# Kernel tuning notes

Hardware: AMD Instinct MI355X
Metric: run time of the kernel (lower is better)

## Reference

```python
import jax, jax.numpy as jnp
import numpy as np

D_MODEL = 1024
N_HEAD = 16
DIM_PER_HEAD = D_MODEL // N_HEAD
B, S = 8, 1024


def setup_inputs() -> dict:
    key = jax.random.key(0)
    ks = jax.random.split(key, 12)
    s = 0.02
    return {
        "k": jax.random.normal(ks[0], (B, S, D_MODEL), jnp.float32),
        "v": jax.random.normal(ks[1], (B, S, D_MODEL), jnp.float32),
        "q": jax.random.normal(ks[2], (B, S, D_MODEL), jnp.float32),
        "attn_mask": jax.random.randint(ks[3], (B, S, S), 0, 2, jnp.int32),
        "Wk": jax.random.normal(ks[4], (D_MODEL, D_MODEL), jnp.float32) * s,
        "bk": jnp.zeros((D_MODEL,), jnp.float32),
        "Wv": jax.random.normal(ks[5], (D_MODEL, D_MODEL), jnp.float32) * s,
        "bv": jnp.zeros((D_MODEL,), jnp.float32),
        "Wq": jax.random.normal(ks[6], (D_MODEL, D_MODEL), jnp.float32) * s,
        "bq": jnp.zeros((D_MODEL,), jnp.float32),
        "Wo": jax.random.normal(ks[7], (D_MODEL, D_MODEL), jnp.float32) * s,
        "bo": jnp.zeros((D_MODEL,), jnp.float32),
    }


def reference(k, v, q, attn_mask, Wk, bk, Wv, bv, Wq, bq, Wo, bo):
    batch, key_len, _ = k.shape
    query_len = q.shape[1]
    scale = 1.0 / jnp.sqrt(jnp.float32(DIM_PER_HEAD))

    def split_heads(x):  # [b, s, d] -> [b, h, s, dh]
        return x.reshape(batch, -1, N_HEAD, DIM_PER_HEAD).transpose(0, 2, 1, 3)

    key_up = split_heads(k @ Wk + bk)
    value_up = split_heads(v @ Wv + bv)
    query_up = split_heads(q @ Wq + bq) * scale

    # [b, h, q, k] scores; mask nonzero entries with -inf (masked_fill_ semantics)
    scores = jnp.einsum("bhqd,bhkd->bhqk", query_up, key_up)
    scores = jnp.where(attn_mask[:, None, :, :] != 0, -jnp.inf, scores)
    attn = jax.nn.softmax(scores, axis=-1)
    # NOTE: original applies dropout but discards the result; attn (pre-dropout) is used.
    context = jnp.einsum("bhqk,bhkd->bhqd", attn, value_up)
    context = context.transpose(0, 2, 1, 3).reshape(batch, query_len, D_MODEL)
    output = context @ Wo + bo
    attn_mean = attn.sum(axis=1) / N_HEAD  # [b, q, k]
    return output, attn_mean
```

## Files before the change

kernel.cpp:

```cpp
#include <hip/hip_runtime.h>
#include <hip/hip_bf16.h>

typedef unsigned short u16;
typedef unsigned int u32;
typedef __attribute__((ext_vector_type(8))) short bf16x8;
typedef __attribute__((ext_vector_type(4))) float f32x4;
typedef __attribute__((ext_vector_type(4))) u16 u16x4;
typedef __attribute__((ext_vector_type(4))) u32 u32x4;

#define DEV static __device__ __forceinline__

DEV u16 f2bf(float x) {
  unsigned u = __builtin_bit_cast(unsigned, x);
  u += 0x7fffu + ((u >> 16) & 1u);
  return (u16)(u >> 16);
}
DEV float bf2f(u16 u) { return __builtin_bit_cast(float, ((unsigned)u) << 16); }

DEV u32 cvtpk(float lo, float hi) {
  u32 r;
  asm("v_cvt_pk_bf16_f32 %0, %1, %2" : "=v"(r) : "v"(lo), "v"(hi));
  return r;
}

DEV void glds16(const u16* g, u16* l) {
  __builtin_amdgcn_global_load_lds(
      (const __attribute__((address_space(1))) void*)g,
      (__attribute__((address_space(3))) void*)l, 16, 0, 0);
}

__global__ __launch_bounds__(256) void xcvt(
    const float* __restrict__ k, const float* __restrict__ v,
    const float* __restrict__ q, u16* __restrict__ Xb) {
  const size_t i0 = (size_t)blockIdx.x * 256 + threadIdx.x;
  for (size_t t = i0; t < 6291456; t += 524288) {
    const size_t e = t * 4;
    const float* src = (e < 8388608) ? k + e
                     : (e < 16777216) ? v + (e - 8388608)
                     : q + (e - 16777216);
    const f32x4 x = *(const f32x4*)src;
    u16x4 o;
#pragma unroll
    for (int r = 0; r < 4; ++r) o[r] = f2bf(x[r]);
    *(u16x4*)&Xb[e] = o;
  }
}

__global__ __launch_bounds__(256) void transpose_w(
    const float* __restrict__ w0, const float* __restrict__ w1,
    const float* __restrict__ w2, const float* __restrict__ w3,
    u16* __restrict__ out) {
  __shared__ u16 tile[32][33];
  const int mat = blockIdx.y;
  const float* in = (mat == 0) ? w0 : (mat == 1) ? w1 : (mat == 2) ? w2 : w3;
  u16* o = out + (size_t)mat * 1048576;
  const int bk = ((int)blockIdx.x & 31) << 5;
  const int bn = ((int)blockIdx.x >> 5) << 5;
  const int tx = threadIdx.x & 31, ty = threadIdx.x >> 5;
#pragma unroll
  for (int i = 0; i < 32; i += 8)
    tile[ty + i][tx] = f2bf(in[(size_t)(bk + ty + i) * 1024 + bn + tx]);
  __syncthreads();
#pragma unroll
  for (int i = 0; i < 32; i += 8)
    o[(size_t)(bn + ty + i) * 1024 + bk + tx] = tile[tx][ty + i];
}

__global__ __launch_bounds__(256) void maskpack(
    const int* __restrict__ mask, unsigned long long* __restrict__ Mb) {
  const int qt = blockIdx.x, b = blockIdx.y;
  const int tid = threadIdx.x;
  const int w = tid >> 6, l = tid & 63;
  const int ln = l & 15, lg = l >> 4;
  const int* Mp = mask + ((size_t)b << 20) + ((size_t)(qt << 4) << 10);
  unsigned long long m = 0ull;
#pragma unroll
  for (int t = 0; t < 16; ++t) {
    const int key = (w << 8) + (t << 4) + ln;
#pragma unroll
    for (int r = 0; r < 4; ++r) {
      const int row = (lg << 2) + r;
      if (Mp[((size_t)row << 10) + key] != 0) m |= 1ull << ((t << 2) + r);
    }
  }
  Mb[((((size_t)b << 6) + qt) << 8) + tid] = m;
}

__global__ __launch_bounds__(256) void gemm_qkv(
    const u16* __restrict__ Xb, const u16* __restrict__ WTall,
    const float* __restrict__ bK, const float* __restrict__ bV,
    const float* __restrict__ bQ,
    u16* __restrict__ Kup, u16* __restrict__ VupT, u16* __restrict__ Qup) {
  __shared__ u16 As[4096];
  __shared__ u16 Bs[4096];
  const int mode = blockIdx.y;
  const u16* A = Xb + (size_t)mode * 8388608;
  const u16* Bw = WTall + (size_t)mode * 1048576;
  const float* bias = (mode == 0) ? bK : (mode == 1) ? bV : bQ;

  const int tid = threadIdx.x;
  const int w = tid >> 6, l = tid & 63;
  const int ln = l & 15, lg = l >> 4, kg8 = lg << 3;
  const int wr = w >> 1, wc = w & 1;
  const int mb = ((int)blockIdx.x >> 3) << 7;
  const int nb = ((int)blockIdx.x & 7) << 7;

  const int srow = (w << 5) + (l >> 2);
  const int sseg = (l & 3) << 3;
  const u16* Ag0 = A + (size_t)(mb + srow) * 1024 + sseg;
  const u16* Bg0 = Bw + (size_t)(nb + srow) * 1024 + sseg;
  u16* Al0 = As + srow * 32 + sseg;
  u16* Bl0 = Bs + srow * 32 + sseg;

  f32x4 acc[4][4] = {};
  const int ar = (wr << 6) + ln;
  const int br = (wc << 6) + ln;

  for (int k0 = 0; k0 < 1024; k0 += 32) {
    glds16(Ag0 + k0, Al0);
    glds16(Ag0 + 16384 + k0, Al0 + 512);
    glds16(Bg0 + k0, Bl0);
    glds16(Bg0 + 16384 + k0, Bl0 + 512);
    __syncthreads();
    bf16x8 aa[4], bb[4];
#pragma unroll
    for (int mt = 0; mt < 4; ++mt) aa[mt] = *(const bf16x8*)&As[(ar + (mt << 4)) * 32 + kg8];
#pragma unroll
    for (int nt = 0; nt < 4; ++nt) bb[nt] = *(const bf16x8*)&Bs[(br + (nt << 4)) * 32 + kg8];
#pragma unroll
    for (int mt = 0; mt < 4; ++mt)
#pragma unroll
      for (int nt = 0; nt < 4; ++nt)
        acc[mt][nt] = __builtin_amdgcn_mfma_f32_16x16x32_bf16(aa[mt], bb[nt], acc[mt][nt], 0, 0, 0);
    __syncthreads();
  }

  const float scale = (mode == 2) ? 0.125f : 1.0f;
#pragma unroll
  for (int mt = 0; mt < 4; ++mt) {
    const int m0 = mb + (wr << 6) + (mt << 4) + (lg << 2);
    const int bb_ = m0 >> 10, s0 = m0 & 1023;
#pragma unroll
    for (int nt = 0; nt < 4; ++nt) {
      const int n = nb + (wc << 6) + (nt << 4) + ln;
      const float bval = bias[n];
      const int h = n >> 6, dh = n & 63;
      const size_t bh = (size_t)(bb_ * 16 + h);
      if (mode == 1) {
        const int wv = dh >> 4, lnv = dh & 15;
        const int kk = s0 >> 5, lgv = (s0 >> 3) & 3, e0 = s0 & 7;
        u16x4 pk;
#pragma unroll
        for (int r = 0; r < 4; ++r) pk[r] = f2bf(acc[mt][nt][r] + bval);
        *(u16x4*)&VupT[(bh << 16) + (wv << 14) + (kk << 9) + (lgv << 7) +
                       (lnv << 3) + e0] = pk;
      } else if (mode == 0) {
        const int half = dh >> 5, lg2 = (dh >> 3) & 3, e = dh & 7;
        const int T = s0 >> 4;
        u16* base = Kup + (bh << 16) + (T << 10) + (half << 9) + (lg2 << 7) + e;
#pragma unroll
        for (int r = 0; r < 4; ++r)
          base[((s0 & 15) + r) << 3] = f2bf(acc[mt][nt][r] + bval);
      } else {
#pragma unroll
        for (int r = 0; r < 4; ++r)
          Qup[((bh << 10) + s0 + r) * 64 + dh] =
              f2bf((acc[mt][nt][r] + bval) * scale);
      }
    }
  }
}

__global__ __launch_bounds__(256) void gemm_out(
    const u16* __restrict__ Ctx, const u16* __restrict__ WTall,
    const float* __restrict__ bO, float* __restrict__ Out) {
  __shared__ u16 As[4096];
  __shared__ u16 Bs[4096];
  const u16* Bw = WTall + 3145728;

  const int tid = threadIdx.x;
  const int w = tid >> 6, l = tid & 63;
  const int ln = l & 15, lg = l >> 4, kg8 = lg << 3;
  const int wr = w >> 1, wc = w & 1;
  const int mb = ((int)blockIdx.x >> 3) << 7;
  const int nb = ((int)blockIdx.x & 7) << 7;

  const int srow = (w << 5) + (l >> 2);
  const int sseg = (l & 3) << 3;
  const u16* Ag0 = Ctx + (size_t)(mb + srow) * 1024 + sseg;
  const u16* Bg0 = Bw + (size_t)(nb + srow) * 1024 + sseg;
  u16* Al0 = As + srow * 32 + sseg;
  u16* Bl0 = Bs + srow * 32 + sseg;

  f32x4 acc[4][4] = {};
  const int ar = (wr << 6) + ln;
  const int br = (wc << 6) + ln;

  for (int k0 = 0; k0 < 1024; k0 += 32) {
    glds16(Ag0 + k0, Al0);
    glds16(Ag0 + 16384 + k0, Al0 + 512);
    glds16(Bg0 + k0, Bl0);
    glds16(Bg0 + 16384 + k0, Bl0 + 512);
    __syncthreads();
    bf16x8 aa[4], bb[4];
#pragma unroll
    for (int mt = 0; mt < 4; ++mt) aa[mt] = *(const bf16x8*)&As[(ar + (mt << 4)) * 32 + kg8];
#pragma unroll
    for (int nt = 0; nt < 4; ++nt) bb[nt] = *(const bf16x8*)&Bs[(br + (nt << 4)) * 32 + kg8];
#pragma unroll
    for (int mt = 0; mt < 4; ++mt)
#pragma unroll
      for (int nt = 0; nt < 4; ++nt)
        acc[mt][nt] = __builtin_amdgcn_mfma_f32_16x16x32_bf16(aa[mt], bb[nt], acc[mt][nt], 0, 0, 0);
    __syncthreads();
  }
#pragma unroll
  for (int mt = 0; mt < 4; ++mt) {
    const int m0 = mb + (wr << 6) + (mt << 4) + (lg << 2);
#pragma unroll
    for (int nt = 0; nt < 4; ++nt) {
      const int n = nb + (wc << 6) + (nt << 4) + ln;
      const float bval = bO[n];
#pragma unroll
      for (int r = 0; r < 4; ++r)
        Out[(size_t)(m0 + r) * 1024 + n] = acc[mt][nt][r] + bval;
    }
  }
}

__global__ __launch_bounds__(256, 2) void attn_kernel(
    const u16* __restrict__ Qup, const u16* __restrict__ Kf,
    const u16* __restrict__ Vf, const unsigned long long* __restrict__ Mb,
    u16* __restrict__ Ctx, float* __restrict__ Am) {
  __shared__ u16 P_lds[16 * 1024];
  __shared__ float red_s[4][16];
  __shared__ float invs[16];

  const int tid = threadIdx.x;
  const int w = tid >> 6, l = tid & 63;
  const int ln = l & 15, lg = l >> 4;
  const int kg8 = lg << 3;

  const int bid = (int)blockIdx.x;
  const int b = bid & 7;
  const int qt = bid >> 3;
  const int qb = qt << 4;

  const unsigned long long mbits = Mb[((((size_t)b << 6) + qt) << 8) + tid];

  u32x4 accp[8];

#pragma unroll 1
  for (int hh = 0; hh < 16; ++hh) {
    const size_t bh = (size_t)(b * 16 + hh);
    const u16* Qp = Qup + ((bh << 10) + qb) * 64;
    const u16* Kb = Kf + (bh << 16);
    const u16* Vb = Vf + (bh << 16) + ((size_t)w << 14);

    const bf16x8 qa0 = *(const bf16x8*)&Qp[ln * 64 + kg8];
    const bf16x8 qa1 = *(const bf16x8*)&Qp[ln * 64 + 32 + kg8];

    bf16x8 ka[3], kb[3];
#pragma unroll
    for (int p = 0; p < 3; ++p) {
      const int To = ((w << 4) + p) << 10;
      ka[p] = *(const bf16x8*)&Kb[To + (l << 3)];
      kb[p] = *(const bf16x8*)&Kb[To + 512 + (l << 3)];
    }

    float rsum[4] = {0, 0, 0, 0};
#pragma unroll
    for (int t = 0; t < 16; ++t) {
      const int s = t % 3;
      const bf16x8 k0 = ka[s], k1 = kb[s];
      if (t + 3 < 16) {
        const int To = ((w << 4) + t + 3) << 10;
        ka[s] = *(const bf16x8*)&Kb[To + (l << 3)];
        kb[s] = *(const bf16x8*)&Kb[To + 512 + (l << 3)];
      }
      f32x4 c = {0, 0, 0, 0};
      c = __builtin_amdgcn_mfma_f32_16x16x32_bf16(qa0, k0, c, 0, 0, 0);
      c = __builtin_amdgcn_mfma_f32_16x16x32_bf16(qa1, k1, c, 0, 0, 0);
      const int key = (w << 8) + (t << 4) + ln;
      float p[4];
#pragma unroll
      for (int r = 0; r < 4; ++r) {
        p[r] = ((mbits >> ((t << 2) + r)) & 1ull) ? 0.0f : __expf(c[r] - 4.0f);
        rsum[r] += p[r];
      }
      const u32 pk01 = cvtpk(p[0], p[1]);
      const u32 pk23 = cvtpk(p[2], p[3]);
      const int r0 = lg << 2;
      *(u16*)((char*)P_lds + ((((r0 + 0) << 11) + (key << 1)) ^ (((r0 + 0) & 7) << 4))) = (u16)pk01;
      *(u16*)((char*)P_lds + ((((r0 + 1) << 11) + (key << 1)) ^ (((r0 + 1) & 7) << 4))) = (u16)(pk01 >> 16);
      *(u16*)((char*)P_lds + ((((r0 + 2) << 11) + (key << 1)) ^ (((r0 + 2) & 7) << 4))) = (u16)pk23;
      *(u16*)((char*)P_lds + ((((r0 + 3) << 11) + (key << 1)) ^ (((r0 + 3) & 7) << 4))) = (u16)(pk23 >> 16);
    }
#pragma unroll
    for (int off = 1; off < 16; off <<= 1) {
#pragma unroll
      for (int r = 0; r < 4; ++r) rsum[r] += __shfl_xor(rsum[r], off);
    }
    if (ln == 0) {
#pragma unroll
      for (int r = 0; r < 4; ++r) red_s[w][(lg << 2) + r] = rsum[r];
    }

    bf16x8 vr[4];
#pragma unroll
    for (int p = 0; p < 4; ++p)
      vr[p] = *(const bf16x8*)&Vb[(p << 9) + (l << 3)];

    __syncthreads();
    float inv[4];
#pragma unroll
    for (int r = 0; r < 4; ++r) {
      const int row = (lg << 2) + r;
      inv[r] = 1.0f / (red_s[0][row] + red_s[1][row] + red_s[2][row] + red_s[3][row]);
    }
    if (ln == 0) {
#pragma unroll
      for (int r = 0; r < 4; ++r) invs[(lg << 2) + r] = inv[r];
    }

    f32x4 c0 = {0, 0, 0, 0}, c1 = {0, 0, 0, 0};
#pragma unroll
    for (int kk = 0; kk < 32; ++kk) {
      const int s = kk & 3;
      const bf16x8 vb = vr[s];
      if (kk + 4 < 32)
        vr[s] = *(const bf16x8*)&Vb[((kk + 4) << 9) + (l << 3)];
      const int a0 = ((ln << 11) + (((kk << 5) + kg8) << 1)) ^ ((ln & 7) << 4);
      const bf16x8 pa = *(const bf16x8*)((const char*)P_lds + a0);
      if (kk & 1)
        c1 = __builtin_amdgcn_mfma_f32_16x16x32_bf16(pa, vb, c1, 0, 0, 0);
      else
        c0 = __builtin_amdgcn_mfma_f32_16x16x32_bf16(pa, vb, c0, 0, 0, 0);
    }
    {
      const u32 q01 = cvtpk((c0[0] + c1[0]) * inv[0], (c0[1] + c1[1]) * inv[1]);
      const u32 q23 = cvtpk((c0[2] + c1[2]) * inv[2], (c0[3] + c1[3]) * inv[3]);
      u16* Cp = &Ctx[(((size_t)b << 10) + qb + (lg << 2)) * 1024 + (hh << 6) + (w << 4) + ln];
      Cp[0] = (u16)q01;
      Cp[1024] = (u16)(q01 >> 16);
      Cp[2048] = (u16)q23;
      Cp[3072] = (u16)(q23 >> 16);
    }

    {
      const int row = tid >> 4;
      const float iv = invs[row];
#pragma unroll
      for (int i = 0; i < 8; ++i) {
        const int chunk = (tid & 15) + (i << 4);
        const int bo_ = ((row << 11) + (chunk << 4)) ^ ((row & 7) << 4);
        const u32x4 pu = *(const u32x4*)((const char*)P_lds + bo_);
        u32x4 o;
#pragma unroll
        for (int j = 0; j < 4; ++j) {
          const float plo = __builtin_bit_cast(float, pu[j] << 16) * iv;
          const float phi = __builtin_bit_cast(float, pu[j] & 0xFFFF0000u) * iv;
          if (hh == 0) {
            o[j] = cvtpk(plo, phi);
          } else {
            const u32 a = accp[i][j];
            const float alo = __builtin_bit_cast(float, a << 16);
            const float ahi = __builtin_bit_cast(float, a & 0xFFFF0000u);
            o[j] = cvtpk(alo + plo, ahi + phi);
          }
        }
        accp[i] = o;
      }
    }
    __syncthreads();
  }

  {
    const int row = tid >> 4;
    float* Ag = Am + (((size_t)b << 10) + qb + row) * 1024;
#pragma unroll
    for (int i = 0; i < 8; ++i) {
      const int chunk = (tid & 15) + (i << 4);
      f32x4 o0, o1;
#pragma unroll
      for (int j = 0; j < 4; ++j) {
        const float lo = __builtin_bit_cast(float, accp[i][j] << 16) * 0.0625f;
        const float hi = __builtin_bit_cast(float, accp[i][j] & 0xFFFF0000u) * 0.0625f;
        if (j < 2) { o0[2 * j] = lo; o0[2 * j + 1] = hi; }
        else       { o1[2 * (j - 2)] = lo; o1[2 * (j - 2) + 1] = hi; }
      }
      *(f32x4*)&Ag[chunk << 3] = o0;
      *(f32x4*)&Ag[(chunk << 3) + 4] = o1;
    }
  }
}

extern "C" void kernel_launch(void* const* d_in, const int* in_sizes, int n_in,
                              void* d_out, int out_size, void* d_ws, size_t ws_size,
                              hipStream_t stream) {
  const float* k_in = (const float*)d_in[0];
  const float* v_in = (const float*)d_in[1];
  const float* q_in = (const float*)d_in[2];
  const int* mask = (const int*)d_in[3];
  const float* Wk = (const float*)d_in[4];
  const float* bk = (const float*)d_in[5];
  const float* Wv = (const float*)d_in[6];
  const float* bv = (const float*)d_in[7];
  const float* Wq = (const float*)d_in[8];
  const float* bq = (const float*)d_in[9];
  const float* Wo = (const float*)d_in[10];
  const float* bo = (const float*)d_in[11];

  float* out = (float*)d_out;
  float* amean = out + (size_t)8 * 1024 * 1024;

  u16* ws = (u16*)d_ws;
  u16* WT = ws;
  u16* Xb = ws + 4194304;
  unsigned long long* Mb = (unsigned long long*)(ws + 29360128);
  u16* Kf   = ws + 71303168;
  u16* Vf   = ws + 79691776;
  u16* Qup  = ws + 88080384;
  u16* Ctx  = ws + 96468992;

  xcvt<<<2048, 256, 0, stream>>>(k_in, v_in, q_in, Xb);
  transpose_w<<<dim3(1024, 4), dim3(256), 0, stream>>>(Wk, Wv, Wq, Wo, WT);
  maskpack<<<dim3(64, 8), dim3(256), 0, stream>>>(mask, Mb);
  gemm_qkv<<<dim3(512, 3), dim3(256), 0, stream>>>(
      Xb, WT, bk, bv, bq, Kf, Vf, Qup);
  attn_kernel<<<dim3(512), dim3(256), 0, stream>>>(
      Qup, Kf, Vf, Mb, Ctx, amean);
  gemm_out<<<512, 256, 0, stream>>>(Ctx, WT, bo, out);
}
```

Baseline: 297.1 us.

## Double-buffer P in LDS and prefetch next head's K/Q across iterations

The per-head probability tile, row sums and inverse sums now live in two alternating LDS buffers. This allows the trailing block barrier at the end of each head iteration to be removed. The next head's K and Q fragments are loaded before the mid-iteration barrier, so their global latency overlaps with the PV phase. The PV MFMA loop is also wrapped in raised wave priority. The cost is LDS use doubling to about 64KB per block and more live registers, which may limit occupancy under the two-blocks-per-CU launch bound.

```diff
diff --git a/kernel.cpp b/kernel.cpp
--- a/kernel.cpp
+++ b/kernel.cpp
@@ -232,9 +232,9 @@
     const u16* __restrict__ Qup, const u16* __restrict__ Kf,
     const u16* __restrict__ Vf, const unsigned long long* __restrict__ Mb,
     u16* __restrict__ Ctx, float* __restrict__ Am) {
-  __shared__ u16 P_lds[16 * 1024];
-  __shared__ float red_s[4][16];
-  __shared__ float invs[16];
+  __shared__ u16 P_lds[2][16384];
+  __shared__ float red_s[2][4][16];
+  __shared__ float invs[2][16];
 
   const int tid = threadIdx.x;
   const int w = tid >> 6, l = tid & 63;
@@ -250,23 +250,27 @@
 
   u32x4 accp[8];
 
+  bf16x8 ka[3], kb[3], qa0, qa1;
+  {
+    const size_t bh0 = (size_t)(b * 16);
+    const u16* Kb0 = Kf + (bh0 << 16);
+    const u16* Qp0 = Qup + ((bh0 << 10) + qb) * 64;
+#pragma unroll
+    for (int p = 0; p < 3; ++p) {
+      const int To = ((w << 4) + p) << 10;
+      ka[p] = *(const bf16x8*)&Kb0[To + (l << 3)];
+      kb[p] = *(const bf16x8*)&Kb0[To + 512 + (l << 3)];
+    }
+    qa0 = *(const bf16x8*)&Qp0[ln * 64 + kg8];
+    qa1 = *(const bf16x8*)&Qp0[ln * 64 + 32 + kg8];
+  }
+
 #pragma unroll 1
   for (int hh = 0; hh < 16; ++hh) {
+    const int pb_ = hh & 1;
     const size_t bh = (size_t)(b * 16 + hh);
-    const u16* Qp = Qup + ((bh << 10) + qb) * 64;
     const u16* Kb = Kf + (bh << 16);
     const u16* Vb = Vf + (bh << 16) + ((size_t)w << 14);
-
-    const bf16x8 qa0 = *(const bf16x8*)&Qp[ln * 64 + kg8];
-    const bf16x8 qa1 = *(const bf16x8*)&Qp[ln * 64 + 32 + kg8];
-
-    bf16x8 ka[3], kb[3];
-#pragma unroll
-    for (int p = 0; p < 3; ++p) {
-      const int To = ((w << 4) + p) << 10;
-      ka[p] = *(const bf16x8*)&Kb[To + (l << 3)];
-      kb[p] = *(const bf16x8*)&Kb[To + 512 + (l << 3)];
-    }
 
     float rsum[4] = {0, 0, 0, 0};
 #pragma unroll
@@ -291,10 +295,11 @@
       const u32 pk01 = cvtpk(p[0], p[1]);
       const u32 pk23 = cvtpk(p[2], p[3]);
       const int r0 = lg << 2;
-      *(u16*)((char*)P_lds + ((((r0 + 0) << 11) + (key << 1)) ^ (((r0 + 0) & 7) << 4))) = (u16)pk01;
-      *(u16*)((char*)P_lds + ((((r0 + 1) << 11) + (key << 1)) ^ (((r0 + 1) & 7) << 4))) = (u16)(pk01 >> 16);
-      *(u16*)((char*)P_lds + ((((r0 + 2) << 11) + (key << 1)) ^ (((r0 + 2) & 7) << 4))) = (u16)pk23;
-      *(u16*)((char*)P_lds + ((((r0 + 3) << 11) + (key << 1)) ^ (((r0 + 3) & 7) << 4))) = (u16)(pk23 >> 16);
+      char* Pb = (char*)P_lds + (pb_ << 15);
+      *(u16*)(Pb + ((((r0 + 0) << 11) + (key << 1)) ^ (((r0 + 0) & 7) << 4))) = (u16)pk01;
+      *(u16*)(Pb + ((((r0 + 1) << 11) + (key << 1)) ^ (((r0 + 1) & 7) << 4))) = (u16)(pk01 >> 16);
+      *(u16*)(Pb + ((((r0 + 2) << 11) + (key << 1)) ^ (((r0 + 2) & 7) << 4))) = (u16)pk23;
+      *(u16*)(Pb + ((((r0 + 3) << 11) + (key << 1)) ^ (((r0 + 3) & 7) << 4))) = (u16)(pk23 >> 16);
     }
 #pragma unroll
     for (int off = 1; off < 16; off <<= 1) {
@@ -303,7 +308,7 @@
     }
     if (ln == 0) {
 #pragma unroll
-      for (int r = 0; r < 4; ++r) red_s[w][(lg << 2) + r] = rsum[r];
+      for (int r = 0; r < 4; ++r) red_s[pb_][w][(lg << 2) + r] = rsum[r];
     }
 
     bf16x8 vr[4];
@@ -311,19 +316,35 @@
     for (int p = 0; p < 4; ++p)
       vr[p] = *(const bf16x8*)&Vb[(p << 9) + (l << 3)];
 
+    if (hh < 15) {
+      const size_t bhn = bh + 1;
+      const u16* Kbn = Kf + (bhn << 16);
+      const u16* Qpn = Qup + ((bhn << 10) + qb) * 64;
+#pragma unroll
+      for (int p = 0; p < 3; ++p) {
+        const int To = ((w << 4) + p) << 10;
+        ka[p] = *(const bf16x8*)&Kbn[To + (l << 3)];
+        kb[p] = *(const bf16x8*)&Kbn[To + 512 + (l << 3)];
+      }
+      qa0 = *(const bf16x8*)&Qpn[ln * 64 + kg8];
+      qa1 = *(const bf16x8*)&Qpn[ln * 64 + 32 + kg8];
+    }
+
     __syncthreads();
     float inv[4];
 #pragma unroll
     for (int r = 0; r < 4; ++r) {
       const int row = (lg << 2) + r;
-      inv[r] = 1.0f / (red_s[0][row] + red_s[1][row] + red_s[2][row] + red_s[3][row]);
+      inv[r] = 1.0f / (red_s[pb_][0][row] + red_s[pb_][1][row] +
+                       red_s[pb_][2][row] + red_s[pb_][3][row]);
     }
     if (ln == 0) {
 #pragma unroll
-      for (int r = 0; r < 4; ++r) invs[(lg << 2) + r] = inv[r];
+      for (int r = 0; r < 4; ++r) invs[pb_][(lg << 2) + r] = inv[r];
     }
 
     f32x4 c0 = {0, 0, 0, 0}, c1 = {0, 0, 0, 0};
+    __builtin_amdgcn_s_setprio(1);
 #pragma unroll
     for (int kk = 0; kk < 32; ++kk) {
       const int s = kk & 3;
@@ -331,12 +352,13 @@
       if (kk + 4 < 32)
         vr[s] = *(const bf16x8*)&Vb[((kk + 4) << 9) + (l << 3)];
       const int a0 = ((ln << 11) + (((kk << 5) + kg8) << 1)) ^ ((ln & 7) << 4);
-      const bf16x8 pa = *(const bf16x8*)((const char*)P_lds + a0);
+      const bf16x8 pa = *(const bf16x8*)((const char*)P_lds + (pb_ << 15) + a0);
       if (kk & 1)
         c1 = __builtin_amdgcn_mfma_f32_16x16x32_bf16(pa, vb, c1, 0, 0, 0);
       else
         c0 = __builtin_amdgcn_mfma_f32_16x16x32_bf16(pa, vb, c0, 0, 0, 0);
     }
+    __builtin_amdgcn_s_setprio(0);
     {
       const u32 q01 = cvtpk((c0[0] + c1[0]) * inv[0], (c0[1] + c1[1]) * inv[1]);
       const u32 q23 = cvtpk((c0[2] + c1[2]) * inv[2], (c0[3] + c1[3]) * inv[3]);
@@ -349,12 +371,12 @@
 
     {
       const int row = tid >> 4;
-      const float iv = invs[row];
+      const float iv = invs[pb_][row];
 #pragma unroll
       for (int i = 0; i < 8; ++i) {
         const int chunk = (tid & 15) + (i << 4);
         const int bo_ = ((row << 11) + (chunk << 4)) ^ ((row & 7) << 4);
-        const u32x4 pu = *(const u32x4*)((const char*)P_lds + bo_);
+        const u32x4 pu = *(const u32x4*)((const char*)P_lds + (pb_ << 15) + bo_);
         u32x4 o;
 #pragma unroll
         for (int j = 0; j < 4; ++j) {
@@ -372,7 +394,6 @@
         accp[i] = o;
       }
     }
-    __syncthreads();
   }
 
   {
```

After: 326.0 us. +9.7%, slower.

## Split attention heads across two blocks and combine partial attention means

Applied to the files above, without the earlier changes.

Each attention block now processes 8 of the 16 heads rather than all of them, which doubles the grid from 512 to 1024 blocks and gives the 256-CU GPU more parallelism. Each half writes its bf16 partial sum of attention probabilities to a workspace buffer. A new combine kernel adds the two partials, scales by 1/16 and writes the fp32 attn_mean. This trades an extra kernel launch and about 32MB of additional global traffic (write plus read of the partials) for better CU occupancy.

```diff
diff --git a/kernel.cpp b/kernel.cpp
--- a/kernel.cpp
+++ b/kernel.cpp
@@ -231,7 +231,7 @@
 __global__ __launch_bounds__(256, 2) void attn_kernel(
     const u16* __restrict__ Qup, const u16* __restrict__ Kf,
     const u16* __restrict__ Vf, const unsigned long long* __restrict__ Mb,
-    u16* __restrict__ Ctx, float* __restrict__ Am) {
+    u16* __restrict__ Ctx, u16* __restrict__ Pp) {
   __shared__ u16 P_lds[16 * 1024];
   __shared__ float red_s[4][16];
   __shared__ float invs[16];
@@ -243,7 +243,9 @@
 
   const int bid = (int)blockIdx.x;
   const int b = bid & 7;
-  const int qt = bid >> 3;
+  const int idx = bid >> 3;
+  const int qt = idx & 63;
+  const int hs = idx >> 6;
   const int qb = qt << 4;
 
   const unsigned long long mbits = Mb[((((size_t)b << 6) + qt) << 8) + tid];
@@ -251,8 +253,9 @@
   u32x4 accp[8];
 
 #pragma unroll 1
-  for (int hh = 0; hh < 16; ++hh) {
-    const size_t bh = (size_t)(b * 16 + hh);
+  for (int hh = 0; hh < 8; ++hh) {
+    const int h = (hs << 3) + hh;
+    const size_t bh = (size_t)(b * 16 + h);
     const u16* Qp = Qup + ((bh << 10) + qb) * 64;
     const u16* Kb = Kf + (bh << 16);
     const u16* Vb = Vf + (bh << 16) + ((size_t)w << 14);
@@ -340,7 +343,7 @@
     {
       const u32 q01 = cvtpk((c0[0] + c1[0]) * inv[0], (c0[1] + c1[1]) * inv[1]);
       const u32 q23 = cvtpk((c0[2] + c1[2]) * inv[2], (c0[3] + c1[3]) * inv[3]);
-      u16* Cp = &Ctx[(((size_t)b << 10) + qb + (lg << 2)) * 1024 + (hh << 6) + (w << 4) + ln];
+      u16* Cp = &Ctx[(((size_t)b << 10) + qb + (lg << 2)) * 1024 + (h << 6) + (w << 4) + ln];
       Cp[0] = (u16)q01;
       Cp[1024] = (u16)(q01 >> 16);
       Cp[2048] = (u16)q23;
@@ -377,22 +380,29 @@
 
   {
     const int row = tid >> 4;
-    float* Ag = Am + (((size_t)b << 10) + qb + row) * 1024;
+    u16* Pg = Pp + ((size_t)hs << 23) + (((size_t)b << 10) + qb + row) * 1024;
 #pragma unroll
     for (int i = 0; i < 8; ++i) {
       const int chunk = (tid & 15) + (i << 4);
-      f32x4 o0, o1;
-#pragma unroll
-      for (int j = 0; j < 4; ++j) {
-        const float lo = __builtin_bit_cast(float, accp[i][j] << 16) * 0.0625f;
-        const float hi = __builtin_bit_cast(float, accp[i][j] & 0xFFFF0000u) * 0.0625f;
-        if (j < 2) { o0[2 * j] = lo; o0[2 * j + 1] = hi; }
-        else       { o1[2 * (j - 2)] = lo; o1[2 * (j - 2) + 1] = hi; }
-      }
-      *(f32x4*)&Ag[chunk << 3] = o0;
-      *(f32x4*)&Ag[(chunk << 3) + 4] = o1;
-    }
-  }
+      *(u32x4*)&Pg[chunk << 3] = accp[i];
+    }
+  }
+}
+
+__global__ __launch_bounds__(256) void combine2(
+    const u16* __restrict__ Pp, float* __restrict__ Am) {
+  const size_t i = ((size_t)blockIdx.x * 256 + threadIdx.x) * 8;
+  const u16x4* q0 = (const u16x4*)&Pp[i];
+  const u16x4* q1 = (const u16x4*)&Pp[8388608 + i];
+  const u16x4 a0 = q0[0], a1 = q0[1], b0 = q1[0], b1 = q1[1];
+  f32x4 lo, hi;
+#pragma unroll
+  for (int r = 0; r < 4; ++r) {
+    lo[r] = (bf2f(a0[r]) + bf2f(b0[r])) * 0.0625f;
+    hi[r] = (bf2f(a1[r]) + bf2f(b1[r])) * 0.0625f;
+  }
+  *(f32x4*)&Am[i] = lo;
+  *(f32x4*)&Am[i + 4] = hi;
 }
 
 extern "C" void kernel_launch(void* const* d_in, const int* in_sizes, int n_in,
@@ -418,6 +428,7 @@
   u16* WT = ws;
   u16* Xb = ws + 4194304;
   unsigned long long* Mb = (unsigned long long*)(ws + 29360128);
+  u16* Pp = ws + 37748736;
   u16* Kf   = ws + 71303168;
   u16* Vf   = ws + 79691776;
   u16* Qup  = ws + 88080384;
@@ -428,7 +439,8 @@
   maskpack<<<dim3(64, 8), dim3(256), 0, stream>>>(mask, Mb);
   gemm_qkv<<<dim3(512, 3), dim3(256), 0, stream>>>(
       Xb, WT, bk, bv, bq, Kf, Vf, Qup);
-  attn_kernel<<<dim3(512), dim3(256), 0, stream>>>(
-      Qup, Kf, Vf, Mb, Ctx, amean);
+  attn_kernel<<<dim3(1024), dim3(256), 0, stream>>>(
+      Qup, Kf, Vf, Mb, Ctx, Pp);
+  combine2<<<4096, 256, 0, stream>>>(Pp, amean);
   gemm_out<<<512, 256, 0, stream>>>(Ctx, WT, bo, out);
 }
```

Result: slower. 309.3 us (+4.1%).
